# Optimization experiments

Measured on AMD Instinct MI355X. Metric: run time of the kernel, lower is better.

Reference implementation:

```python
import jax, jax.numpy as jnp
import numpy as np

B, C, H, W = 8, 64, 128, 128
OUT, K, PAD = 128, 9, 1  # 3x3 kernel -> K=9 taps


def setup_inputs() -> dict:
    key = jax.random.key(0)
    ks = jax.random.split(key, 6)
    x = jax.random.normal(ks[0], (B, C, H, W), dtype=jnp.float32)
    # trained-like params: small random offsets (std ~1-2 px) and mask logits
    w_offset = jax.random.normal(ks[1], (2 * K, C, 3, 3), dtype=jnp.float32) * 0.05
    b_offset = jax.random.normal(ks[2], (2 * K,), dtype=jnp.float32) * 0.1
    w_mask = jax.random.normal(ks[3], (K, C, 3, 3), dtype=jnp.float32) * 0.05
    b_mask = jax.random.normal(ks[4], (K,), dtype=jnp.float32) * 0.1
    w_conv = jax.random.normal(ks[5], (OUT, C, 3, 3), dtype=jnp.float32) * (1.0 / np.sqrt(C * 9))
    return {"x": x, "w_offset": w_offset, "b_offset": b_offset,
            "w_mask": w_mask, "b_mask": b_mask, "w_conv": w_conv}


def _conv3x3(x, w, b):
    out = jax.lax.conv_general_dilated(
        x, w, window_strides=(1, 1), padding=((PAD, PAD), (PAD, PAD)),
        dimension_numbers=("NCHW", "OIHW", "NCHW"))
    return out + b[None, :, None, None]


def _bilinear_gather(img, gy, gx):
    # img: [C,H,W]; gy,gx: [K,H,W] float sampling coords (zero outside bounds)
    C_, H_, W_ = img.shape
    y0 = jnp.floor(gy)
    x0 = jnp.floor(gx)
    wy = gy - y0
    wx = gx - x0
    img_flat = img.reshape(C_, H_ * W_)

    def corner(yi, xi, wgt):
        valid = ((yi >= 0) & (yi < H_) & (xi >= 0) & (xi < W_)).astype(img.dtype)
        yc = jnp.clip(yi, 0, H_ - 1).astype(jnp.int32)
        xc = jnp.clip(xi, 0, W_ - 1).astype(jnp.int32)
        v = img_flat[:, yc * W_ + xc]  # [C,K,H,W]
        return v * (wgt * valid)[None]

    return (corner(y0, x0, (1 - wy) * (1 - wx))
            + corner(y0, x0 + 1, (1 - wy) * wx)
            + corner(y0 + 1, x0, wy * (1 - wx))
            + corner(y0 + 1, x0 + 1, wy * wx))  # [C,K,H,W]


def reference(x, w_offset, b_offset, w_mask, b_mask, w_conv):
    offset = _conv3x3(x, w_offset, b_offset)                  # [B,18,H,W]
    mask = jax.nn.sigmoid(_conv3x3(x, w_mask, b_mask))        # [B,9,H,W]
    B_, C_, H_, W_ = x.shape
    # torchvision layout: channel 2k = dy, 2k+1 = dx for kernel tap k
    off = offset.reshape(B_, K, 2, H_, W_)
    dy, dx = off[:, :, 0], off[:, :, 1]                       # [B,K,H,W]
    ky, kx = jnp.meshgrid(jnp.arange(3, dtype=x.dtype),
                          jnp.arange(3, dtype=x.dtype), indexing="ij")
    gy = jnp.arange(H_, dtype=x.dtype)[None, None, :, None] - PAD + ky.reshape(1, K, 1, 1) + dy
    gx = jnp.arange(W_, dtype=x.dtype)[None, None, None, :] - PAD + kx.reshape(1, K, 1, 1) + dx
    sampled = jax.vmap(_bilinear_gather)(x, gy, gx)           # [B,C,K,H,W]
    sampled = sampled * mask[:, None]                         # modulated (DCNv2)
    out = jnp.einsum("bckhw,ock->bohw", sampled, w_conv.reshape(OUT, C_, K))
    return out
```

## Files before the change

### kernel.cpp

```cpp
#include <hip/hip_runtime.h>
#include <math.h>

#define Himg 128
#define Wimg 128
#define HW   16384
#define Cin  64
#define Kk   9
#define OUTC 128
#define Bsz  8

typedef __attribute__((ext_vector_type(8))) _Float16 half8;
typedef __attribute__((ext_vector_type(4))) float   floatx4;
typedef __attribute__((ext_vector_type(4))) int     intx4;

#define SPL8(v) ((half8){(v),(v),(v),(v),(v),(v),(v),(v)})

__global__ __launch_bounds__(256) void prep(const float* __restrict__ x,
                                            const float* __restrict__ w_conv,
                                            const float* __restrict__ w_offset,
                                            const float* __restrict__ w_mask,
                                            _Float16* __restrict__ xt,
                                            _Float16* __restrict__ wpk_h,
                                            _Float16* __restrict__ wpk2) {
    __shared__ _Float16 tile[Cin][130];
    int t   = threadIdx.x;
    int bid = blockIdx.x;

    if (bid < 1024) {
        int b = bid >> 7;
        int h = bid & 127;
        const float* xb = x + (size_t)b * Cin * HW + (size_t)h * Wimg;
#pragma unroll
        for (int j = 0; j < 32; ++j) {
            int e = t + j * 256;
            int c = e >> 7;
            int w = e & 127;
            tile[c][w] = (_Float16)xb[(size_t)c * HW + w];
        }
        __syncthreads();
        unsigned* dst = (unsigned*)xt + ((size_t)b * HW + (size_t)h * Wimg) * 32;
#pragma unroll
        for (int j = 0; j < 16; ++j) {
            int d  = t + j * 256;
            int w  = d >> 5;
            int cp = d & 31;
            union { unsigned u; _Float16 hh[2]; } pk;
            pk.hh[0] = tile[2 * cp][w];
            pk.hh[1] = tile[2 * cp + 1][w];
            dst[d] = pk.u;
        }
        return;
    }

    if (bid < 1024 + 288) {
        int idx = (bid - 1024) * 256 + t;
        if (idx < Kk * Cin * OUTC) {
            int i    = idx & 7;
            int l    = (idx >> 3) & 63;
            int g    = idx >> 9;
            int mt   = g & 7;
            int ch   = g >> 3;
            int kq   = l >> 4;
            int ln16 = l & 15;
            int o    = mt * 16 + ln16;
            int kl   = kq * 8 + i;
            int c    = (ch & 1) * 32 + kl;
            int kt   = ch >> 1;
            wpk_h[idx] = (_Float16)w_conv[(o * Cin + c) * 9 + kt];
        }
        return;
    }

    {
        int idx = (bid - 1312) * 256 + t;
        if (idx < 18 * 32 * 32) {
            int i    = idx & 7;
            int l    = (idx >> 3) & 63;
            int g    = idx >> 9;
            int mt0  = g & 1;
            int ch   = g >> 1;
            int kq   = l >> 4;
            int ln16 = l & 15;
            int m    = mt0 * 16 + ln16;
            int kl   = kq * 8 + i;
            int c    = (ch & 1) * 32 + kl;
            int kt   = ch >> 1;
            float v = 0.0f;
            if (m < 18)      v = w_offset[(m * Cin + c) * 9 + kt];
            else if (m < 27) v = w_mask[((m - 18) * Cin + c) * 9 + kt];
            wpk2[idx] = (_Float16)v;
        }
    }
}

__global__ __launch_bounds__(256, 2) void deform_fused(
        const _Float16* __restrict__ xt, const _Float16* __restrict__ wpk_h,
        const _Float16* __restrict__ wpk2,
        const float* __restrict__ b_offset, const float* __restrict__ b_mask,
        float* __restrict__ out) {
    __shared__ _Float16 Vw[4][2][32][40];
    __shared__ float    Pw[4][32][32];
    __shared__ int      Geo[4][9][32][4];

    int t    = threadIdx.x;
    int bid  = blockIdx.x;
    int b    = bid & 7;
    int pb   = bid >> 3;
    int pix0 = pb << 7;
    int h    = pb;

    int lane = t & 63;
    int wv   = t >> 6;
    int qloc = lane >> 2;
    int c4   = lane & 3;
    int kq   = lane >> 4;
    int ln16 = lane & 15;
    int sp0  = wv * 32;

    const _Float16* xtb  = xt + (size_t)b * HW * Cin;
    const half8* wsrc    = (const half8*)wpk_h;
    const half8* w2src   = (const half8*)wpk2;

    floatx4 acc2_00 = (floatx4){0.f,0.f,0.f,0.f};
    floatx4 acc2_10 = (floatx4){0.f,0.f,0.f,0.f};
    floatx4 acc2_01 = (floatx4){0.f,0.f,0.f,0.f};
    floatx4 acc2_11 = (floatx4){0.f,0.f,0.f,0.f};

    half8 pvA0, pvB0, pvA1, pvB1, af0p, af1p;

#define LOADX0(chn, g, DST) { \
    const int ktn = (chn) >> 1, cgn = (chn) & 1; \
    int row = h + (ktn / 3) - 1; \
    int col = sp0 + (g) * 16 + qloc + (ktn % 3) - 1; \
    bool okc = (row >= 0) && (row < Himg) && (col >= 0) && (col < Wimg); \
    if (okc) DST = *(const half8*)(xtb + ((size_t)(row * Wimg + col)) * Cin \
                                   + cgn * 32 + c4 * 8); \
    else     DST = SPL8((_Float16)0.0f); \
}

#define P0STEP(ch, PV0, PV1) { \
    half8 af0c = af0p, af1c = af1p; \
    *(half8*)&Vw[wv][(ch) & 1][qloc][c4 * 8]      = PV0; \
    *(half8*)&Vw[wv][(ch) & 1][16 + qloc][c4 * 8] = PV1; \
    if ((ch) < 16) { LOADX0((ch) + 2, 0, PV0) LOADX0((ch) + 2, 1, PV1) } \
    if ((ch) < 17) { \
        af0p = w2src[((size_t)((ch) + 1) * 2 + 0) * 64 + lane]; \
        af1p = w2src[((size_t)((ch) + 1) * 2 + 1) * 64 + lane]; \
    } \
    half8 bf0 = *(const half8*)&Vw[wv][(ch) & 1][ln16][kq * 8]; \
    half8 bf1 = *(const half8*)&Vw[wv][(ch) & 1][16 + ln16][kq * 8]; \
    acc2_00 = __builtin_amdgcn_mfma_f32_16x16x32_f16(af0c, bf0, acc2_00, 0, 0, 0); \
    acc2_10 = __builtin_amdgcn_mfma_f32_16x16x32_f16(af1c, bf0, acc2_10, 0, 0, 0); \
    acc2_01 = __builtin_amdgcn_mfma_f32_16x16x32_f16(af0c, bf1, acc2_01, 0, 0, 0); \
    acc2_11 = __builtin_amdgcn_mfma_f32_16x16x32_f16(af1c, bf1, acc2_11, 0, 0, 0); \
}

    LOADX0(0, 0, pvA0) LOADX0(0, 1, pvA1)
    LOADX0(1, 0, pvB0) LOADX0(1, 1, pvB1)
    af0p = w2src[(size_t)0 * 64 + lane];
    af1p = w2src[(size_t)1 * 64 + lane];

    P0STEP(0,  pvA0, pvA1) P0STEP(1,  pvB0, pvB1)
    P0STEP(2,  pvA0, pvA1) P0STEP(3,  pvB0, pvB1)
    P0STEP(4,  pvA0, pvA1) P0STEP(5,  pvB0, pvB1)
    P0STEP(6,  pvA0, pvA1) P0STEP(7,  pvB0, pvB1)
    P0STEP(8,  pvA0, pvA1) P0STEP(9,  pvB0, pvB1)
    P0STEP(10, pvA0, pvA1) P0STEP(11, pvB0, pvB1)
    P0STEP(12, pvA0, pvA1) P0STEP(13, pvB0, pvB1)
    P0STEP(14, pvA0, pvA1) P0STEP(15, pvB0, pvB1)
    P0STEP(16, pvA0, pvA1) P0STEP(17, pvB0, pvB1)

#pragma unroll
    for (int r = 0; r < 4; ++r) {
        Pw[wv][kq * 4 + r][ln16]           = acc2_00[r];
        Pw[wv][16 + kq * 4 + r][ln16]      = acc2_10[r];
        Pw[wv][kq * 4 + r][16 + ln16]      = acc2_01[r];
        Pw[wv][16 + kq * 4 + r][16 + ln16] = acc2_11[r];
    }

    {
        int pxg = lane >> 1;
        float fh = (float)h, fw = (float)(sp0 + pxg);
#pragma unroll
        for (int k = 0; k < 9; ++k) {
            float dyv = Pw[wv][2 * k][pxg]     + b_offset[2 * k];
            float dxv = Pw[wv][2 * k + 1][pxg] + b_offset[2 * k + 1];
            float mz  = Pw[wv][18 + k][pxg]    + b_mask[k];
            float mkv = 1.0f / (1.0f + expf(-mz));

            float gy  = fh + (float)(k / 3) - 1.0f + dyv;
            float gx  = fw + (float)(k % 3) - 1.0f + dxv;
            float y0f = floorf(gy), x0f = floorf(gx);
            int   y0  = (int)y0f,   x0 = (int)x0f;
            float wy  = gy - y0f,   wx = gx - x0f;
            int   y1  = y0 + 1,     x1 = x0 + 1;

            bool vy0 = (y0 >= 0) && (y0 < Himg);
            bool vy1 = (y1 >= 0) && (y1 < Himg);
            bool vx0 = (x0 >= 0) && (x0 < Wimg);
            bool vx1 = (x1 >= 0) && (x1 < Wimg);

            float w00 = (vy0 && vx0) ? (1.0f - wy) * (1.0f - wx) * mkv : 0.0f;
            float w01 = (vy0 && vx1) ? (1.0f - wy) * wx          * mkv : 0.0f;
            float w10 = (vy1 && vx0) ? wy          * (1.0f - wx) * mkv : 0.0f;
            float w11 = (vy1 && vx1) ? wy          * wx          * mkv : 0.0f;

            int y0c = min(max(y0, 0), Himg - 1), y1c = min(max(y1, 0), Himg - 1);
            int x0c = min(max(x0, 0), Wimg - 1), x1c = min(max(x1, 0), Wimg - 1);
            int geom = (y0c * Wimg + x0c) | ((x1c - x0c) << 14) | ((y1c - y0c) << 15);
            union { unsigned u; _Float16 hh[2]; } pk;
            int wabk, wcdk;
            pk.hh[0] = (_Float16)w00; pk.hh[1] = (_Float16)w01; wabk = (int)pk.u;
            pk.hh[0] = (_Float16)w10; pk.hh[1] = (_Float16)w11; wcdk = (int)pk.u;
            if ((lane & 1) == 0) {
                Geo[wv][k][pxg][0] = geom;
                Geo[wv][k][pxg][1] = wabk;
                Geo[wv][k][pxg][2] = wcdk;
            }
        }
    }

    floatx4 acc[8][2];
#pragma unroll
    for (int i = 0; i < 8; ++i) {
        acc[i][0] = (floatx4){0.f,0.f,0.f,0.f};
        acc[i][1] = (floatx4){0.f,0.f,0.f,0.f};
    }

    half8 gA0, gA1, gA2, gA3;
    half8 gB0, gB1, gB2, gB3;
    half8 gC0, gC1, gC2, gC3;
    half8 gD0, gD1, gD2, gD3;

#define LOADG(chn, g, D0, D1, D2, D3) { \
    int gg = Geo[wv][(chn) >> 1][(g) * 16 + qloc][0]; \
    const _Float16* xc = xtb + (size_t)(gg & 0x3fff) * Cin \
                         + ((chn) & 1) * 32 + c4 * 8; \
    int ob = (gg & 0x4000) >> 8;    \
    int oc = (gg & 0x8000) >> 2;    \
    D0 = *(const half8*)(xc); \
    D1 = *(const half8*)(xc + ob); \
    D2 = *(const half8*)(xc + oc); \
    D3 = *(const half8*)(xc + oc + ob); \
}

#define P1STEP(ch, A0, A1, A2, A3, C0, C1, C2, C3) { \
     \
    half8 w_0 = wsrc[((size_t)(ch) * 8 + 0) * 64 + lane]; \
    half8 w_1 = wsrc[((size_t)(ch) * 8 + 1) * 64 + lane]; \
    half8 w_2 = wsrc[((size_t)(ch) * 8 + 2) * 64 + lane]; \
    half8 w_3 = wsrc[((size_t)(ch) * 8 + 3) * 64 + lane]; \
    half8 w_4 = wsrc[((size_t)(ch) * 8 + 4) * 64 + lane]; \
    half8 w_5 = wsrc[((size_t)(ch) * 8 + 5) * 64 + lane]; \
    half8 w_6 = wsrc[((size_t)(ch) * 8 + 6) * 64 + lane]; \
    half8 w_7 = wsrc[((size_t)(ch) * 8 + 7) * 64 + lane]; \
     \
    intx4 q0 = *(const intx4*)&Geo[wv][(ch) >> 1][qloc][0]; \
    intx4 q1 = *(const intx4*)&Geo[wv][(ch) >> 1][16 + qloc][0]; \
    union { unsigned u; _Float16 hh[2]; } u1, u2; \
    u1.u = (unsigned)q0.y;  u2.u = (unsigned)q0.z; \
    half8 vv0 = A0 * SPL8(u1.hh[0]) + A1 * SPL8(u1.hh[1]) \
              + A2 * SPL8(u2.hh[0]) + A3 * SPL8(u2.hh[1]); \
    *(half8*)&Vw[wv][(ch) & 1][qloc][c4 * 8] = vv0; \
    u1.u = (unsigned)q1.y;  u2.u = (unsigned)q1.z; \
    half8 vv1 = C0 * SPL8(u1.hh[0]) + C1 * SPL8(u1.hh[1]) \
              + C2 * SPL8(u2.hh[0]) + C3 * SPL8(u2.hh[1]); \
    *(half8*)&Vw[wv][(ch) & 1][16 + qloc][c4 * 8] = vv1; \
     \
    if ((ch) < 16) { \
        LOADG((ch) + 2, 0, A0, A1, A2, A3) \
        LOADG((ch) + 2, 1, C0, C1, C2, C3) \
    } \
    half8 bf0 = *(const half8*)&Vw[wv][(ch) & 1][ln16][kq * 8]; \
    half8 bf1 = *(const half8*)&Vw[wv][(ch) & 1][16 + ln16][kq * 8]; \
    acc[0][0] = __builtin_amdgcn_mfma_f32_16x16x32_f16(w_0, bf0, acc[0][0], 0, 0, 0); \
    acc[1][0] = __builtin_amdgcn_mfma_f32_16x16x32_f16(w_1, bf0, acc[1][0], 0, 0, 0); \
    acc[2][0] = __builtin_amdgcn_mfma_f32_16x16x32_f16(w_2, bf0, acc[2][0], 0, 0, 0); \
    acc[3][0] = __builtin_amdgcn_mfma_f32_16x16x32_f16(w_3, bf0, acc[3][0], 0, 0, 0); \
    acc[4][0] = __builtin_amdgcn_mfma_f32_16x16x32_f16(w_4, bf0, acc[4][0], 0, 0, 0); \
    acc[5][0] = __builtin_amdgcn_mfma_f32_16x16x32_f16(w_5, bf0, acc[5][0], 0, 0, 0); \
    acc[6][0] = __builtin_amdgcn_mfma_f32_16x16x32_f16(w_6, bf0, acc[6][0], 0, 0, 0); \
    acc[7][0] = __builtin_amdgcn_mfma_f32_16x16x32_f16(w_7, bf0, acc[7][0], 0, 0, 0); \
    acc[0][1] = __builtin_amdgcn_mfma_f32_16x16x32_f16(w_0, bf1, acc[0][1], 0, 0, 0); \
    acc[1][1] = __builtin_amdgcn_mfma_f32_16x16x32_f16(w_1, bf1, acc[1][1], 0, 0, 0); \
    acc[2][1] = __builtin_amdgcn_mfma_f32_16x16x32_f16(w_2, bf1, acc[2][1], 0, 0, 0); \
    acc[3][1] = __builtin_amdgcn_mfma_f32_16x16x32_f16(w_3, bf1, acc[3][1], 0, 0, 0); \
    acc[4][1] = __builtin_amdgcn_mfma_f32_16x16x32_f16(w_4, bf1, acc[4][1], 0, 0, 0); \
    acc[5][1] = __builtin_amdgcn_mfma_f32_16x16x32_f16(w_5, bf1, acc[5][1], 0, 0, 0); \
    acc[6][1] = __builtin_amdgcn_mfma_f32_16x16x32_f16(w_6, bf1, acc[6][1], 0, 0, 0); \
    acc[7][1] = __builtin_amdgcn_mfma_f32_16x16x32_f16(w_7, bf1, acc[7][1], 0, 0, 0); \
}

    LOADG(0, 0, gA0, gA1, gA2, gA3)
    LOADG(0, 1, gC0, gC1, gC2, gC3)
    LOADG(1, 0, gB0, gB1, gB2, gB3)
    LOADG(1, 1, gD0, gD1, gD2, gD3)

    P1STEP(0,  gA0, gA1, gA2, gA3, gC0, gC1, gC2, gC3)
    P1STEP(1,  gB0, gB1, gB2, gB3, gD0, gD1, gD2, gD3)
    P1STEP(2,  gA0, gA1, gA2, gA3, gC0, gC1, gC2, gC3)
    P1STEP(3,  gB0, gB1, gB2, gB3, gD0, gD1, gD2, gD3)
    P1STEP(4,  gA0, gA1, gA2, gA3, gC0, gC1, gC2, gC3)
    P1STEP(5,  gB0, gB1, gB2, gB3, gD0, gD1, gD2, gD3)
    P1STEP(6,  gA0, gA1, gA2, gA3, gC0, gC1, gC2, gC3)
    P1STEP(7,  gB0, gB1, gB2, gB3, gD0, gD1, gD2, gD3)
    P1STEP(8,  gA0, gA1, gA2, gA3, gC0, gC1, gC2, gC3)
    P1STEP(9,  gB0, gB1, gB2, gB3, gD0, gD1, gD2, gD3)
    P1STEP(10, gA0, gA1, gA2, gA3, gC0, gC1, gC2, gC3)
    P1STEP(11, gB0, gB1, gB2, gB3, gD0, gD1, gD2, gD3)
    P1STEP(12, gA0, gA1, gA2, gA3, gC0, gC1, gC2, gC3)
    P1STEP(13, gB0, gB1, gB2, gB3, gD0, gD1, gD2, gD3)
    P1STEP(14, gA0, gA1, gA2, gA3, gC0, gC1, gC2, gC3)
    P1STEP(15, gB0, gB1, gB2, gB3, gD0, gD1, gD2, gD3)
    P1STEP(16, gA0, gA1, gA2, gA3, gC0, gC1, gC2, gC3)
    P1STEP(17, gB0, gB1, gB2, gB3, gD0, gD1, gD2, gD3)

#pragma unroll
    for (int mt = 0; mt < 8; ++mt) {
#pragma unroll
        for (int g = 0; g < 2; ++g) {
#pragma unroll
            for (int r = 0; r < 4; ++r) {
                int o = mt * 16 + kq * 4 + r;
                out[(size_t)(b * OUTC + o) * HW + pix0 + sp0 + g * 16 + ln16]
                    = acc[mt][g][r];
            }
        }
    }
}

extern "C" void kernel_launch(void* const* d_in, const int* in_sizes, int n_in,
                              void* d_out, int out_size, void* d_ws, size_t ws_size,
                              hipStream_t stream) {
    const float* x        = (const float*)d_in[0];
    const float* w_offset = (const float*)d_in[1];
    const float* b_offset = (const float*)d_in[2];
    const float* w_mask   = (const float*)d_in[3];
    const float* b_mask   = (const float*)d_in[4];
    const float* w_conv   = (const float*)d_in[5];
    float* out = (float*)d_out;

    _Float16* wpk_h = (_Float16*)d_ws;
    _Float16* wpk2  = wpk_h + 73728;
    _Float16* xtb   = wpk2 + 18432;

    prep<<<1384, 256, 0, stream>>>(x, w_conv, w_offset, w_mask, xtb, wpk_h, wpk2);
    deform_fused<<<1024, 256, 0, stream>>>(xtb, wpk_h, wpk2, b_offset, b_mask, out);
}
```

Before: 156.8 us.

## Replace LDS staging with ds_bpermute transposes and raise occupancy to three blocks

The per-wave LDS buffer Vw used to transpose gathered/modulated activations into MFMA B-fragment layout is removed; data is now shuffled across lanes with ds_bpermute instead. The gather prefetch depth in the main MFMA phase drops from two channel-steps to one, halving the live gather registers, and launch bounds rise to 3 blocks per CU. The aim is to cut LDS usage and register pressure so more waves can hide gather latency, at the cost of less prefetch distance and possible spills under the tighter register cap.

```diff
diff --git a/kernel.cpp b/kernel.cpp
--- a/kernel.cpp
+++ b/kernel.cpp
@@ -93,12 +93,11 @@
     }
 }
 
-__global__ __launch_bounds__(256, 2) void deform_fused(
+__global__ __launch_bounds__(256, 3) void deform_fused(
         const _Float16* __restrict__ xt, const _Float16* __restrict__ wpk_h,
         const _Float16* __restrict__ wpk2,
         const float* __restrict__ b_offset, const float* __restrict__ b_mask,
         float* __restrict__ out) {
-    __shared__ _Float16 Vw[4][2][32][40];
     __shared__ float    Pw[4][32][32];
     __shared__ int      Geo[4][9][32][4];
 
@@ -116,10 +115,21 @@
     int kq   = lane >> 4;
     int ln16 = lane & 15;
     int sp0  = wv * 32;
+    int pidx = (ln16 * 4 + kq) * 4;
 
     const _Float16* xtb  = xt + (size_t)b * HW * Cin;
     const half8* wsrc    = (const half8*)wpk_h;
     const half8* w2src   = (const half8*)wpk2;
+
+#define BPERM8(DST, SRC) { \
+    union { half8 h; int d[4]; } _s, _d; \
+    _s.h = SRC; \
+    _d.d[0] = __builtin_amdgcn_ds_bpermute(pidx, _s.d[0]); \
+    _d.d[1] = __builtin_amdgcn_ds_bpermute(pidx, _s.d[1]); \
+    _d.d[2] = __builtin_amdgcn_ds_bpermute(pidx, _s.d[2]); \
+    _d.d[3] = __builtin_amdgcn_ds_bpermute(pidx, _s.d[3]); \
+    DST = _d.h; \
+}
 
     floatx4 acc2_00 = (floatx4){0.f,0.f,0.f,0.f};
     floatx4 acc2_10 = (floatx4){0.f,0.f,0.f,0.f};
@@ -140,15 +150,14 @@
 
 #define P0STEP(ch, PV0, PV1) { \
     half8 af0c = af0p, af1c = af1p; \
-    *(half8*)&Vw[wv][(ch) & 1][qloc][c4 * 8]      = PV0; \
-    *(half8*)&Vw[wv][(ch) & 1][16 + qloc][c4 * 8] = PV1; \
+    half8 bf0, bf1; \
+    BPERM8(bf0, PV0) \
+    BPERM8(bf1, PV1) \
     if ((ch) < 16) { LOADX0((ch) + 2, 0, PV0) LOADX0((ch) + 2, 1, PV1) } \
     if ((ch) < 17) { \
         af0p = w2src[((size_t)((ch) + 1) * 2 + 0) * 64 + lane]; \
         af1p = w2src[((size_t)((ch) + 1) * 2 + 1) * 64 + lane]; \
     } \
-    half8 bf0 = *(const half8*)&Vw[wv][(ch) & 1][ln16][kq * 8]; \
-    half8 bf1 = *(const half8*)&Vw[wv][(ch) & 1][16 + ln16][kq * 8]; \
     acc2_00 = __builtin_amdgcn_mfma_f32_16x16x32_f16(af0c, bf0, acc2_00, 0, 0, 0); \
     acc2_10 = __builtin_amdgcn_mfma_f32_16x16x32_f16(af1c, bf0, acc2_10, 0, 0, 0); \
     acc2_01 = __builtin_amdgcn_mfma_f32_16x16x32_f16(af0c, bf1, acc2_01, 0, 0, 0); \
@@ -227,10 +236,7 @@
         acc[i][1] = (floatx4){0.f,0.f,0.f,0.f};
     }
 
-    half8 gA0, gA1, gA2, gA3;
-    half8 gB0, gB1, gB2, gB3;
-    half8 gC0, gC1, gC2, gC3;
-    half8 gD0, gD1, gD2, gD3;
+    half8 g0, g1, g2, g3, g4, g5, g6, g7;
 
 #define LOADG(chn, g, D0, D1, D2, D3) { \
     int gg = Geo[wv][(chn) >> 1][(g) * 16 + qloc][0]; \
@@ -244,7 +250,7 @@
     D3 = *(const half8*)(xc + oc + ob); \
 }
 
-#define P1STEP(ch, A0, A1, A2, A3, C0, C1, C2, C3) { \
+#define P1STEP(ch) { \
      \
     half8 w_0 = wsrc[((size_t)(ch) * 8 + 0) * 64 + lane]; \
     half8 w_1 = wsrc[((size_t)(ch) * 8 + 1) * 64 + lane]; \
@@ -259,20 +265,20 @@
     intx4 q1 = *(const intx4*)&Geo[wv][(ch) >> 1][16 + qloc][0]; \
     union { unsigned u; _Float16 hh[2]; } u1, u2; \
     u1.u = (unsigned)q0.y;  u2.u = (unsigned)q0.z; \
-    half8 vv0 = A0 * SPL8(u1.hh[0]) + A1 * SPL8(u1.hh[1]) \
-              + A2 * SPL8(u2.hh[0]) + A3 * SPL8(u2.hh[1]); \
-    *(half8*)&Vw[wv][(ch) & 1][qloc][c4 * 8] = vv0; \
+    half8 vv0 = g0 * SPL8(u1.hh[0]) + g1 * SPL8(u1.hh[1]) \
+              + g2 * SPL8(u2.hh[0]) + g3 * SPL8(u2.hh[1]); \
     u1.u = (unsigned)q1.y;  u2.u = (unsigned)q1.z; \
-    half8 vv1 = C0 * SPL8(u1.hh[0]) + C1 * SPL8(u1.hh[1]) \
-              + C2 * SPL8(u2.hh[0]) + C3 * SPL8(u2.hh[1]); \
-    *(half8*)&Vw[wv][(ch) & 1][16 + qloc][c4 * 8] = vv1; \
+    half8 vv1 = g4 * SPL8(u1.hh[0]) + g5 * SPL8(u1.hh[1]) \
+              + g6 * SPL8(u2.hh[0]) + g7 * SPL8(u2.hh[1]); \
      \
-    if ((ch) < 16) { \
-        LOADG((ch) + 2, 0, A0, A1, A2, A3) \
-        LOADG((ch) + 2, 1, C0, C1, C2, C3) \
+    if ((ch) < 17) { \
+        LOADG((ch) + 1, 0, g0, g1, g2, g3) \
+        LOADG((ch) + 1, 1, g4, g5, g6, g7) \
     } \
-    half8 bf0 = *(const half8*)&Vw[wv][(ch) & 1][ln16][kq * 8]; \
-    half8 bf1 = *(const half8*)&Vw[wv][(ch) & 1][16 + ln16][kq * 8]; \
+     \
+    half8 bf0, bf1; \
+    BPERM8(bf0, vv0) \
+    BPERM8(bf1, vv1) \
     acc[0][0] = __builtin_amdgcn_mfma_f32_16x16x32_f16(w_0, bf0, acc[0][0], 0, 0, 0); \
     acc[1][0] = __builtin_amdgcn_mfma_f32_16x16x32_f16(w_1, bf0, acc[1][0], 0, 0, 0); \
     acc[2][0] = __builtin_amdgcn_mfma_f32_16x16x32_f16(w_2, bf0, acc[2][0], 0, 0, 0); \
@@ -291,29 +297,14 @@
     acc[7][1] = __builtin_amdgcn_mfma_f32_16x16x32_f16(w_7, bf1, acc[7][1], 0, 0, 0); \
 }
 
-    LOADG(0, 0, gA0, gA1, gA2, gA3)
-    LOADG(0, 1, gC0, gC1, gC2, gC3)
-    LOADG(1, 0, gB0, gB1, gB2, gB3)
-    LOADG(1, 1, gD0, gD1, gD2, gD3)
-
-    P1STEP(0,  gA0, gA1, gA2, gA3, gC0, gC1, gC2, gC3)
-    P1STEP(1,  gB0, gB1, gB2, gB3, gD0, gD1, gD2, gD3)
-    P1STEP(2,  gA0, gA1, gA2, gA3, gC0, gC1, gC2, gC3)
-    P1STEP(3,  gB0, gB1, gB2, gB3, gD0, gD1, gD2, gD3)
-    P1STEP(4,  gA0, gA1, gA2, gA3, gC0, gC1, gC2, gC3)
-    P1STEP(5,  gB0, gB1, gB2, gB3, gD0, gD1, gD2, gD3)
-    P1STEP(6,  gA0, gA1, gA2, gA3, gC0, gC1, gC2, gC3)
-    P1STEP(7,  gB0, gB1, gB2, gB3, gD0, gD1, gD2, gD3)
-    P1STEP(8,  gA0, gA1, gA2, gA3, gC0, gC1, gC2, gC3)
-    P1STEP(9,  gB0, gB1, gB2, gB3, gD0, gD1, gD2, gD3)
-    P1STEP(10, gA0, gA1, gA2, gA3, gC0, gC1, gC2, gC3)
-    P1STEP(11, gB0, gB1, gB2, gB3, gD0, gD1, gD2, gD3)
-    P1STEP(12, gA0, gA1, gA2, gA3, gC0, gC1, gC2, gC3)
-    P1STEP(13, gB0, gB1, gB2, gB3, gD0, gD1, gD2, gD3)
-    P1STEP(14, gA0, gA1, gA2, gA3, gC0, gC1, gC2, gC3)
-    P1STEP(15, gB0, gB1, gB2, gB3, gD0, gD1, gD2, gD3)
-    P1STEP(16, gA0, gA1, gA2, gA3, gC0, gC1, gC2, gC3)
-    P1STEP(17, gB0, gB1, gB2, gB3, gD0, gD1, gD2, gD3)
+    LOADG(0, 0, g0, g1, g2, g3)
+    LOADG(0, 1, g4, g5, g6, g7)
+
+    P1STEP(0)  P1STEP(1)  P1STEP(2)  P1STEP(3)
+    P1STEP(4)  P1STEP(5)  P1STEP(6)  P1STEP(7)
+    P1STEP(8)  P1STEP(9)  P1STEP(10) P1STEP(11)
+    P1STEP(12) P1STEP(13) P1STEP(14) P1STEP(15)
+    P1STEP(16) P1STEP(17)
 
 #pragma unroll
     for (int mt = 0; mt < 8; ++mt) {
```

New measurement: 162.9 us. +3.9%, slower.

## Stage conv weights in double-buffered LDS shared across waves

Applied to the files above, without the earlier changes.

Replaces per-wave global loads of the main-conv weight fragments with a cooperative block-wide load into a double-buffered LDS region that aliases the offset/mask scratch buffer. Each channel step writes the next chunk's weights to LDS and prefetches the one after from global into registers. The aim is to cut redundant global/L2 weight traffic, since all four waves previously loaded the same weights. In exchange it adds a block barrier per step and LDS read traffic, which can stall waves and weaken latency hiding.

```diff
diff --git a/kernel.cpp b/kernel.cpp
--- a/kernel.cpp
+++ b/kernel.cpp
@@ -99,7 +99,10 @@
         const float* __restrict__ b_offset, const float* __restrict__ b_mask,
         float* __restrict__ out) {
     __shared__ _Float16 Vw[4][2][32][40];
-    __shared__ float    Pw[4][32][32];
+    __shared__ union PWU {
+        float    P[4][32][32];
+        _Float16 Wl[2][4096];
+    } pwu;
     __shared__ int      Geo[4][9][32][4];
 
     int t    = threadIdx.x;
@@ -120,6 +123,8 @@
     const _Float16* xtb  = xt + (size_t)b * HW * Cin;
     const half8* wsrc    = (const half8*)wpk_h;
     const half8* w2src   = (const half8*)wpk2;
+
+#define BAR() asm volatile("s_waitcnt lgkmcnt(0)\n\ts_barrier" ::: "memory");
 
     floatx4 acc2_00 = (floatx4){0.f,0.f,0.f,0.f};
     floatx4 acc2_10 = (floatx4){0.f,0.f,0.f,0.f};
@@ -172,10 +177,10 @@
 
 #pragma unroll
     for (int r = 0; r < 4; ++r) {
-        Pw[wv][kq * 4 + r][ln16]           = acc2_00[r];
-        Pw[wv][16 + kq * 4 + r][ln16]      = acc2_10[r];
-        Pw[wv][kq * 4 + r][16 + ln16]      = acc2_01[r];
-        Pw[wv][16 + kq * 4 + r][16 + ln16] = acc2_11[r];
+        pwu.P[wv][kq * 4 + r][ln16]           = acc2_00[r];
+        pwu.P[wv][16 + kq * 4 + r][ln16]      = acc2_10[r];
+        pwu.P[wv][kq * 4 + r][16 + ln16]      = acc2_01[r];
+        pwu.P[wv][16 + kq * 4 + r][16 + ln16] = acc2_11[r];
     }
 
     {
@@ -183,9 +188,9 @@
         float fh = (float)h, fw = (float)(sp0 + pxg);
 #pragma unroll
         for (int k = 0; k < 9; ++k) {
-            float dyv = Pw[wv][2 * k][pxg]     + b_offset[2 * k];
-            float dxv = Pw[wv][2 * k + 1][pxg] + b_offset[2 * k + 1];
-            float mz  = Pw[wv][18 + k][pxg]    + b_mask[k];
+            float dyv = pwu.P[wv][2 * k][pxg]     + b_offset[2 * k];
+            float dxv = pwu.P[wv][2 * k + 1][pxg] + b_offset[2 * k + 1];
+            float mz  = pwu.P[wv][18 + k][pxg]    + b_mask[k];
             float mkv = 1.0f / (1.0f + expf(-mz));
 
             float gy  = fh + (float)(k / 3) - 1.0f + dyv;
@@ -231,6 +236,7 @@
     half8 gB0, gB1, gB2, gB3;
     half8 gC0, gC1, gC2, gC3;
     half8 gD0, gD1, gD2, gD3;
+    half8 wrA, wrB;
 
 #define LOADG(chn, g, D0, D1, D2, D3) { \
     int gg = Geo[wv][(chn) >> 1][(g) * 16 + qloc][0]; \
@@ -244,16 +250,27 @@
     D3 = *(const half8*)(xc + oc + ob); \
 }
 
+#define LOADW(chn) { \
+    wrA = wsrc[(size_t)(chn) * 512 + t]; \
+    wrB = wsrc[(size_t)(chn) * 512 + 256 + t]; \
+}
+
 #define P1STEP(ch, A0, A1, A2, A3, C0, C1, C2, C3) { \
      \
-    half8 w_0 = wsrc[((size_t)(ch) * 8 + 0) * 64 + lane]; \
-    half8 w_1 = wsrc[((size_t)(ch) * 8 + 1) * 64 + lane]; \
-    half8 w_2 = wsrc[((size_t)(ch) * 8 + 2) * 64 + lane]; \
-    half8 w_3 = wsrc[((size_t)(ch) * 8 + 3) * 64 + lane]; \
-    half8 w_4 = wsrc[((size_t)(ch) * 8 + 4) * 64 + lane]; \
-    half8 w_5 = wsrc[((size_t)(ch) * 8 + 5) * 64 + lane]; \
-    half8 w_6 = wsrc[((size_t)(ch) * 8 + 6) * 64 + lane]; \
-    half8 w_7 = wsrc[((size_t)(ch) * 8 + 7) * 64 + lane]; \
+    half8 w_0 = *(const half8*)&pwu.Wl[(ch) & 1][0 * 512 + lane * 8]; \
+    half8 w_1 = *(const half8*)&pwu.Wl[(ch) & 1][1 * 512 + lane * 8]; \
+    half8 w_2 = *(const half8*)&pwu.Wl[(ch) & 1][2 * 512 + lane * 8]; \
+    half8 w_3 = *(const half8*)&pwu.Wl[(ch) & 1][3 * 512 + lane * 8]; \
+    half8 w_4 = *(const half8*)&pwu.Wl[(ch) & 1][4 * 512 + lane * 8]; \
+    half8 w_5 = *(const half8*)&pwu.Wl[(ch) & 1][5 * 512 + lane * 8]; \
+    half8 w_6 = *(const half8*)&pwu.Wl[(ch) & 1][6 * 512 + lane * 8]; \
+    half8 w_7 = *(const half8*)&pwu.Wl[(ch) & 1][7 * 512 + lane * 8]; \
+     \
+    if ((ch) < 17) { \
+        *(half8*)&pwu.Wl[((ch) + 1) & 1][t * 8]        = wrA; \
+        *(half8*)&pwu.Wl[((ch) + 1) & 1][2048 + t * 8] = wrB; \
+    } \
+    if ((ch) < 16) LOADW((ch) + 2) \
      \
     intx4 q0 = *(const intx4*)&Geo[wv][(ch) >> 1][qloc][0]; \
     intx4 q1 = *(const intx4*)&Geo[wv][(ch) >> 1][16 + qloc][0]; \
@@ -289,12 +306,19 @@
     acc[5][1] = __builtin_amdgcn_mfma_f32_16x16x32_f16(w_5, bf1, acc[5][1], 0, 0, 0); \
     acc[6][1] = __builtin_amdgcn_mfma_f32_16x16x32_f16(w_6, bf1, acc[6][1], 0, 0, 0); \
     acc[7][1] = __builtin_amdgcn_mfma_f32_16x16x32_f16(w_7, bf1, acc[7][1], 0, 0, 0); \
-}
-
+    if ((ch) < 17) BAR() \
+}
+
+    LOADW(0)
     LOADG(0, 0, gA0, gA1, gA2, gA3)
     LOADG(0, 1, gC0, gC1, gC2, gC3)
     LOADG(1, 0, gB0, gB1, gB2, gB3)
     LOADG(1, 1, gD0, gD1, gD2, gD3)
+    BAR()
+    *(half8*)&pwu.Wl[0][t * 8]        = wrA;
+    *(half8*)&pwu.Wl[0][2048 + t * 8] = wrB;
+    LOADW(1)
+    BAR()
 
     P1STEP(0,  gA0, gA1, gA2, gA3, gC0, gC1, gC2, gC3)
     P1STEP(1,  gB0, gB1, gB2, gB3, gD0, gD1, gD2, gD3)
```

Result: slower. 176.7 us (+12.7%).
